# Kernel optimization log

Measured on AMD Instinct MI355X. Metric: run time of the kernel, lower is better.

The kernel has to match this reference:

```python
import jax, jax.numpy as jnp
import numpy as np

EPS = 1e-06

def phi(x):
    # canonical linear-attention feature map: elu(x) + 1 (positive features)
    return jax.nn.elu(x) + 1.0

def setup_inputs() -> dict:
    key = jax.random.key(0)
    kq, kk, kv = jax.random.split(key, 3)
    B, H, S, D = 4, 16, 4096, 64
    query = jax.random.normal(kq, (B, H, S, D), dtype=jnp.float32)
    k = jax.random.normal(kk, (B, H, S, D), dtype=jnp.float32)
    value = jax.random.normal(kv, (B, H, S, D), dtype=jnp.float32)
    attention_mask = jnp.ones((B, S), dtype=jnp.float32)
    return {"query": query, "key": k, "value": value, "attention_mask": attention_mask}

def reference(query, key, value, attention_mask):
    B, H, S, D = query.shape
    q = query / jnp.sqrt(jnp.asarray(D, query.dtype))
    phi_q = phi(q)                                   # [b,h,n,d]
    phi_k = phi(key)                                 # [b,h,n,d]
    mask = attention_mask[:, None, :, None].astype(phi_k.dtype)  # [b,1,n,1]
    phi_k = phi_k * mask
    kv_term = jnp.einsum('bhnd,bhnv->bhdv', phi_k, value)        # [b,h,d,v]
    output = jnp.einsum('bhnd,bhdv->bhnv', phi_q, kv_term)       # [b,h,n,v]
    k_one = jnp.sum(phi_k, axis=2)                               # [b,h,d] == phi_k @ masked ones
    normalizer = jnp.einsum('bhnd,bhd->bhn', phi_q, k_one)[..., None]  # [b,h,n,1]
    return output / (normalizer + EPS)
```

## Files before the change

kernel.cpp:

```cpp
#include <hip/hip_runtime.h>

typedef unsigned short ushort_t;
typedef unsigned int uint32;
typedef __bf16 bf16x8 __attribute__((ext_vector_type(8)));
typedef float f32x4 __attribute__((ext_vector_type(4)));

#define NB 4
#define NH 16
#define NS 4096
#define ND 64
#define NBH 64
#define EPSF 1e-6f

#define CH1 16
#define ROWS1 (NS / CH1)
#define P2R 64
#define LDJ 72
#define LDJW 36
#define BTSZ (80 * 64)

__device__ __forceinline__ float phi_f(float x) {
    return x > 0.0f ? x + 1.0f : __expf(x);
}
__device__ __forceinline__ ushort_t bf16_rn(float x) {
    uint32 u = __float_as_uint(x);
    uint32 r = (u + 0x7FFFu + ((u >> 16) & 1u)) >> 16;
    return (ushort_t)r;
}
__device__ __forceinline__ void split2(float x, ushort_t& h, ushort_t& l) {
    h = bf16_rn(x);
    float hf = __uint_as_float(((uint32)h) << 16);
    l = bf16_rn(x - hf);
}
union FragP { ushort_t s[8]; bf16x8 v; };
__device__ __forceinline__ bf16x8 ld_frag(const ushort_t* arr, int widx) {
    return *(const bf16x8*)((const uint32*)arr + widx);
}
__device__ __forceinline__ f32x4 mfma16(bf16x8 a, bf16x8 b, f32x4 c) {
    return __builtin_amdgcn_mfma_f32_16x16x32_bf16(a, b, c, 0, 0, 0);
}

template<bool PART>
__global__ __launch_bounds__(512, 8)
void la_pass1(const float* __restrict__ Kin, const float* __restrict__ Vin,
              const float* __restrict__ Min, float* __restrict__ okv,
              float* __restrict__ ok1)
{
    const int t  = threadIdx.x;
    const int cx = blockIdx.x;
    const int bh = blockIdx.y;
    const int bb = bh >> 4;
    const float* Kb = Kin + (long long)bh * NS * ND;
    const float* Vb = Vin + (long long)bh * NS * ND;
    const float* Mb = Min + (long long)bb * NS;

    __shared__ __align__(16) ushort_t skh[64 * LDJ], skl[64 * LDJ];
    __shared__ __align__(16) ushort_t svh[64 * LDJ], svl[64 * LDJ];

    const int p  = t & 31;
    const int c0 = (t >> 5) * 4;
    const int wv = t >> 6;
    const int ds = wv >> 1;
    const int nb = (wv & 1) * 2;
    const int m  = t & 15;
    const int q  = (t & 63) >> 4;

    const f32x4 zf = {0.f, 0.f, 0.f, 0.f};
    f32x4 acc0 = zf, acc1 = zf;
    float k1loc[4] = {0.f, 0.f, 0.f, 0.f};

    const int s0 = cx * ROWS1;

    float4 ka, kc, va, vc;
    float m0, m1;
#define LOADT(tt) { \
        const int r0_ = s0 + (tt) * 64 + 2 * p; \
        const float* kp_ = Kb + (long long)r0_ * ND + c0; \
        const float* vp_ = Vb + (long long)r0_ * ND + c0; \
        ka = *(const float4*)kp_;  kc = *(const float4*)(kp_ + ND); \
        va = *(const float4*)vp_;  vc = *(const float4*)(vp_ + ND); \
        m0 = Mb[r0_]; m1 = Mb[r0_ + 1]; }

    LOADT(0);

    for (int tile = 0; tile < ROWS1 / 64; ++tile) {
        __syncthreads();
        {
            const float kr0[4] = {ka.x, ka.y, ka.z, ka.w};
            const float kr1[4] = {kc.x, kc.y, kc.z, kc.w};
            const float vr0[4] = {va.x, va.y, va.z, va.w};
            const float vr1[4] = {vc.x, vc.y, vc.z, vc.w};
            #pragma unroll
            for (int i = 0; i < 4; ++i) {
                const float x0 = phi_f(kr0[i]) * m0;
                const float x1 = phi_f(kr1[i]) * m1;
                k1loc[i] += x0 + x1;
                ushort_t h0, l0, h1, l1;
                split2(x0, h0, l0); split2(x1, h1, l1);
                const int widx = (c0 + i) * LDJW + p;
                ((uint32*)skh)[widx] = (uint32)h0 | ((uint32)h1 << 16);
                ((uint32*)skl)[widx] = (uint32)l0 | ((uint32)l1 << 16);
                split2(vr0[i], h0, l0); split2(vr1[i], h1, l1);
                ((uint32*)svh)[widx] = (uint32)h0 | ((uint32)h1 << 16);
                ((uint32*)svl)[widx] = (uint32)l0 | ((uint32)l1 << 16);
            }
        }
        if (tile + 1 < ROWS1 / 64) LOADT(tile + 1);
        __syncthreads();
        #pragma unroll
        for (int ks = 0; ks < 2; ++ks) {
            const int fo = ks * 16 + q * 4;
            const bf16x8 ah = ld_frag(skh, (16 * ds + m) * LDJW + fo);
            const bf16x8 al = ld_frag(skl, (16 * ds + m) * LDJW + fo);
            {
                const bf16x8 fbh = ld_frag(svh, (16 * (nb + 0) + m) * LDJW + fo);
                const bf16x8 fbl = ld_frag(svl, (16 * (nb + 0) + m) * LDJW + fo);
                acc0 = mfma16(al, fbh, acc0); acc0 = mfma16(ah, fbl, acc0); acc0 = mfma16(ah, fbh, acc0);
            }
            {
                const bf16x8 fbh = ld_frag(svh, (16 * (nb + 1) + m) * LDJW + fo);
                const bf16x8 fbl = ld_frag(svl, (16 * (nb + 1) + m) * LDJW + fo);
                acc1 = mfma16(al, fbh, acc1); acc1 = mfma16(ah, fbl, acc1); acc1 = mfma16(ah, fbh, acc1);
            }
        }
    }
#undef LOADT

    const int dbase = 16 * ds + q * 4;
    if (PART) {
        float* outp = okv + (long long)(bh * CH1 + cx) * (ND * ND);
        #pragma unroll
        for (int i = 0; i < 4; ++i) {
            outp[(dbase + i) * ND + 16 * (nb + 0) + m] = acc0[i];
            outp[(dbase + i) * ND + 16 * (nb + 1) + m] = acc1[i];
        }
    } else {
        float* outp = okv + (long long)bh * (ND * ND);
        #pragma unroll
        for (int i = 0; i < 4; ++i) {
            atomicAdd(&outp[(dbase + i) * ND + 16 * (nb + 0) + m], acc0[i]);
            atomicAdd(&outp[(dbase + i) * ND + 16 * (nb + 1) + m], acc1[i]);
        }
    }
    __syncthreads();
    float* red = (float*)skh;
    #pragma unroll
    for (int i = 0; i < 4; ++i) red[(c0 + i) * 33 + p] = k1loc[i];
    __syncthreads();
    if (t < 64) {
        float s = 0.f;
        #pragma unroll
        for (int pp = 0; pp < 32; ++pp) s += red[t * 33 + pp];
        if (PART) ok1[(bh * CH1 + cx) * ND + t] = s;
        else      atomicAdd(&ok1[bh * ND + t], s);
    }
}

__global__ __launch_bounds__(256)
void la_reduce(const float* __restrict__ pkv, const float* __restrict__ pk1,
               ushort_t* __restrict__ BTh, ushort_t* __restrict__ BTl)
{
    const int t = threadIdx.x;
    const int bh = blockIdx.x;
    const float4* src = (const float4*)(pkv + (long long)bh * CH1 * ND * ND);
    float4 a[4];
    #pragma unroll
    for (int i = 0; i < 4; ++i) { a[i].x = 0.f; a[i].y = 0.f; a[i].z = 0.f; a[i].w = 0.f; }
    for (int c = 0; c < CH1; ++c) {
        #pragma unroll
        for (int i = 0; i < 4; ++i) {
            const float4 v = src[c * 1024 + t + 256 * i];
            a[i].x += v.x; a[i].y += v.y; a[i].z += v.z; a[i].w += v.w;
        }
    }
    ushort_t* oh = BTh + (long long)bh * BTSZ;
    ushort_t* ol = BTl + (long long)bh * BTSZ;
    #pragma unroll
    for (int i = 0; i < 4; ++i) {
        const int e4 = t + 256 * i;
        const int d  = e4 >> 4;
        const int v0 = (e4 & 15) * 4;
        const float vals[4] = {a[i].x, a[i].y, a[i].z, a[i].w};
        #pragma unroll
        for (int j = 0; j < 4; ++j) {
            ushort_t h, l; split2(vals[j], h, l);
            oh[(v0 + j) * ND + d] = h;
            ol[(v0 + j) * ND + d] = l;
        }
    }
    if (t < ND) {
        float s = 0.f;
        for (int c = 0; c < CH1; ++c) s += pk1[(bh * CH1 + c) * ND + t];
        ushort_t h, l; split2(s, h, l);
        oh[64 * ND + t] = h; ol[64 * ND + t] = l;
    }
    for (int z = t; z < 15 * 64; z += 256) { oh[65 * ND + z] = 0; ol[65 * ND + z] = 0; }
}

__global__ __launch_bounds__(256)
void la_convert(const float* __restrict__ kv, const float* __restrict__ k1,
                ushort_t* __restrict__ BTh, ushort_t* __restrict__ BTl)
{
    const int t = threadIdx.x;
    const int bh = blockIdx.x;
    const float* kvb = kv + (long long)bh * ND * ND;
    ushort_t* oh = BTh + (long long)bh * BTSZ;
    ushort_t* ol = BTl + (long long)bh * BTSZ;
    for (int e = t; e < ND * ND; e += 256) {
        const int d = e >> 6, v = e & 63;
        ushort_t h, l; split2(kvb[e], h, l);
        oh[v * ND + d] = h; ol[v * ND + d] = l;
    }
    if (t < ND) { ushort_t h, l; split2(k1[bh * ND + t], h, l); oh[64 * ND + t] = h; ol[64 * ND + t] = l; }
    for (int z = t; z < 15 * 64; z += 256) { oh[65 * ND + z] = 0; ol[65 * ND + z] = 0; }
}

__global__ __launch_bounds__(256, 6)
void la_pass2(const float* __restrict__ Qin, const ushort_t* __restrict__ BTh,
              const ushort_t* __restrict__ BTl, float* __restrict__ Out)
{
    const int t  = threadIdx.x;
    const int bh = blockIdx.y;
    const int s0 = blockIdx.x * P2R;
    const long long base = (long long)bh * NS * ND;
    const int wv = t >> 6;
    const int m  = t & 15;
    const int q  = (t & 63) >> 4;
    const int lane = t & 63;
    const ushort_t* Bh = BTh + (long long)bh * BTSZ;
    const ushort_t* Bl = BTl + (long long)bh * BTSZ;

    bf16x8 aH[2], aL[2];
    {
        const int row = s0 + 16 * wv + m;
        const float* qp = Qin + base + (long long)row * ND;
        float4 x0[2], x1[2];
        #pragma unroll
        for (int ks = 0; ks < 2; ++ks) {
            x0[ks] = *(const float4*)(qp + ks * 32 + q * 8);
            x1[ks] = *(const float4*)(qp + ks * 32 + q * 8 + 4);
        }
        #pragma unroll
        for (int ks = 0; ks < 2; ++ks) {
            const float xs[8] = {x0[ks].x, x0[ks].y, x0[ks].z, x0[ks].w,
                                 x1[ks].x, x1[ks].y, x1[ks].z, x1[ks].w};
            FragP fh, fl;
            #pragma unroll
            for (int i = 0; i < 8; ++i) {
                ushort_t h, l; split2(phi_f(xs[i] * 0.125f), h, l);
                fh.s[i] = h; fl.s[i] = l;
            }
            aH[ks] = fh.v; aL[ks] = fl.v;
        }
    }

    const f32x4 zf = {0.f, 0.f, 0.f, 0.f};
    f32x4 acc[5];
    #pragma unroll
    for (int b = 0; b < 5; ++b) acc[b] = zf;

    #pragma unroll
    for (int nt = 0; nt < 5; ++nt) {
        #pragma unroll
        for (int ks = 0; ks < 2; ++ks) {
            const int bo = (16 * nt + m) * ND + ks * 32 + q * 8;
            const bf16x8 fbh = *(const bf16x8*)(Bh + bo);
            const bf16x8 fbl = *(const bf16x8*)(Bl + bo);
            acc[nt] = mfma16(aL[ks], fbh, acc[nt]);
            acc[nt] = mfma16(aH[ks], fbl, acc[nt]);
            acc[nt] = mfma16(aH[ks], fbh, acc[nt]);
        }
    }

    float* outb = Out + base;
    const int rbase = s0 + 16 * wv + q * 4;
    #pragma unroll
    for (int i = 0; i < 4; ++i) {
        const float nv = __shfl(acc[4][i], lane & 48, 64);
        const float rn = 1.0f / (nv + EPSF);
        const long long ro = (long long)(rbase + i) * ND;
        outb[ro +  0 + m] = acc[0][i] * rn;
        outb[ro + 16 + m] = acc[1][i] * rn;
        outb[ro + 32 + m] = acc[2][i] * rn;
        outb[ro + 48 + m] = acc[3][i] * rn;
    }
}

extern "C" void kernel_launch(void* const* d_in, const int* in_sizes, int n_in,
                              void* d_out, int out_size, void* d_ws, size_t ws_size,
                              hipStream_t stream)
{
    const float* Q = (const float*)d_in[0];
    const float* K = (const float*)d_in[1];
    const float* V = (const float*)d_in[2];
    const float* M = (const float*)d_in[3];
    float* Out = (float*)d_out;

    const size_t partf = (size_t)NBH * CH1 * ND * ND;
    const size_t pk1f  = (size_t)NBH * CH1 * ND;
    const size_t kvf   = (size_t)NBH * ND * ND;
    const size_t k1f   = (size_t)NBH * ND;
    const size_t btu   = (size_t)NBH * BTSZ;
    const size_t need  = (partf + pk1f) * sizeof(float) + 2 * btu * sizeof(ushort_t);

    if (ws_size >= need) {
        float* PKV = (float*)d_ws;
        float* PK1 = PKV + partf;
        ushort_t* BThp = (ushort_t*)(PK1 + pk1f);
        ushort_t* BTlp = BThp + btu;
        la_pass1<true><<<dim3(CH1, NBH), dim3(512), 0, stream>>>(K, V, M, PKV, PK1);
        la_reduce<<<dim3(NBH), dim3(256), 0, stream>>>(PKV, PK1, BThp, BTlp);
        la_pass2<<<dim3(NS / P2R, NBH), dim3(256), 0, stream>>>(Q, BThp, BTlp, Out);
    } else {
        float* KVb = (float*)d_ws;
        float* K1b = KVb + kvf;
        ushort_t* BThp = (ushort_t*)(K1b + k1f);
        ushort_t* BTlp = BThp + btu;
        hipMemsetAsync(d_ws, 0, (kvf + k1f) * sizeof(float), stream);
        la_pass1<false><<<dim3(CH1, NBH), dim3(512), 0, stream>>>(K, V, M, KVb, K1b);
        la_convert<<<dim3(NBH), dim3(256), 0, stream>>>(KVb, K1b, BThp, BTlp);
        la_pass2<<<dim3(NS / P2R, NBH), dim3(256), 0, stream>>>(Q, BThp, BTlp, Out);
    }
}
```

Measured before the change: 264.9 us.

## Restructure pass1 to 256 threads with four accumulators per wave

```diff
diff --git a/kernel.cpp b/kernel.cpp
--- a/kernel.cpp
+++ b/kernel.cpp
@@ -15,8 +15,8 @@
 #define CH1 16
 #define ROWS1 (NS / CH1)
 #define P2R 64
-#define LDJ 72
-#define LDJW 36
+#define LDJ 70
+#define LDJW 35
 #define BTSZ (80 * 64)
 
 __device__ __forceinline__ float phi_f(float x) {
@@ -32,16 +32,23 @@
     float hf = __uint_as_float(((uint32)h) << 16);
     l = bf16_rn(x - hf);
 }
+union FragU { uint32 u[4]; bf16x8 v; };
+__device__ __forceinline__ bf16x8 ld_frag(const ushort_t* arr, int widx) {
+    const uint32* p = (const uint32*)arr;
+    FragU f;
+    f.u[0] = p[widx]; f.u[1] = p[widx + 1]; f.u[2] = p[widx + 2]; f.u[3] = p[widx + 3];
+    return f.v;
+}
 union FragP { ushort_t s[8]; bf16x8 v; };
-__device__ __forceinline__ bf16x8 ld_frag(const ushort_t* arr, int widx) {
-    return *(const bf16x8*)((const uint32*)arr + widx);
+__device__ __forceinline__ bf16x8 ld_frag16(const ushort_t* arr, int off16) {
+    return *(const bf16x8*)(arr + off16);
 }
 __device__ __forceinline__ f32x4 mfma16(bf16x8 a, bf16x8 b, f32x4 c) {
     return __builtin_amdgcn_mfma_f32_16x16x32_bf16(a, b, c, 0, 0, 0);
 }
 
 template<bool PART>
-__global__ __launch_bounds__(512, 8)
+__global__ __launch_bounds__(256, 4)
 void la_pass1(const float* __restrict__ Kin, const float* __restrict__ Vin,
               const float* __restrict__ Min, float* __restrict__ okv,
               float* __restrict__ ok1)
@@ -57,52 +64,50 @@
     __shared__ __align__(16) ushort_t skh[64 * LDJ], skl[64 * LDJ];
     __shared__ __align__(16) ushort_t svh[64 * LDJ], svl[64 * LDJ];
 
-    const int p  = t & 31;
-    const int c0 = (t >> 5) * 4;
-    const int wv = t >> 6;
-    const int ds = wv >> 1;
-    const int nb = (wv & 1) * 2;
-    const int m  = t & 15;
-    const int q  = (t & 63) >> 4;
+    const int rr0 = t >> 4;
+    const int c   = (t & 15) * 4;
+    const int wv  = t >> 6;
+    const int m   = t & 15;
+    const int q   = (t & 63) >> 4;
 
     const f32x4 zf = {0.f, 0.f, 0.f, 0.f};
-    f32x4 acc0 = zf, acc1 = zf;
+    f32x4 acc0 = zf, acc1 = zf, acc2 = zf, acc3 = zf;
     float k1loc[4] = {0.f, 0.f, 0.f, 0.f};
 
     const int s0 = cx * ROWS1;
 
-    float4 ka, kc, va, vc;
-    float m0, m1;
+    float4 k4[4], v4[4];
+    float  mk[4];
 #define LOADT(tt) { \
-        const int r0_ = s0 + (tt) * 64 + 2 * p; \
-        const float* kp_ = Kb + (long long)r0_ * ND + c0; \
-        const float* vp_ = Vb + (long long)r0_ * ND + c0; \
-        ka = *(const float4*)kp_;  kc = *(const float4*)(kp_ + ND); \
-        va = *(const float4*)vp_;  vc = *(const float4*)(vp_ + ND); \
-        m0 = Mb[r0_]; m1 = Mb[r0_ + 1]; }
+        const long long rb_ = (long long)(s0 + (tt) * 64 + rr0); \
+        const float* kp_ = Kb + rb_ * ND + c; \
+        const float* vp_ = Vb + rb_ * ND + c; \
+        k4[0] = *(const float4*)(kp_);            v4[0] = *(const float4*)(vp_); \
+        k4[1] = *(const float4*)(kp_ + 16 * ND);  v4[1] = *(const float4*)(vp_ + 16 * ND); \
+        k4[2] = *(const float4*)(kp_ + 32 * ND);  v4[2] = *(const float4*)(vp_ + 32 * ND); \
+        k4[3] = *(const float4*)(kp_ + 48 * ND);  v4[3] = *(const float4*)(vp_ + 48 * ND); \
+        mk[0] = Mb[rb_]; mk[1] = Mb[rb_ + 16]; mk[2] = Mb[rb_ + 32]; mk[3] = Mb[rb_ + 48]; }
 
     LOADT(0);
 
     for (int tile = 0; tile < ROWS1 / 64; ++tile) {
         __syncthreads();
-        {
-            const float kr0[4] = {ka.x, ka.y, ka.z, ka.w};
-            const float kr1[4] = {kc.x, kc.y, kc.z, kc.w};
-            const float vr0[4] = {va.x, va.y, va.z, va.w};
-            const float vr1[4] = {vc.x, vc.y, vc.z, vc.w};
+        #pragma unroll
+        for (int j = 0; j < 4; ++j) {
+            const int rr = rr0 + 16 * j;
+            const float xs[4] = {k4[j].x, k4[j].y, k4[j].z, k4[j].w};
+            const float vs[4] = {v4[j].x, v4[j].y, v4[j].z, v4[j].w};
             #pragma unroll
             for (int i = 0; i < 4; ++i) {
-                const float x0 = phi_f(kr0[i]) * m0;
-                const float x1 = phi_f(kr1[i]) * m1;
-                k1loc[i] += x0 + x1;
-                ushort_t h0, l0, h1, l1;
-                split2(x0, h0, l0); split2(x1, h1, l1);
-                const int widx = (c0 + i) * LDJW + p;
-                ((uint32*)skh)[widx] = (uint32)h0 | ((uint32)h1 << 16);
-                ((uint32*)skl)[widx] = (uint32)l0 | ((uint32)l1 << 16);
-                split2(vr0[i], h0, l0); split2(vr1[i], h1, l1);
-                ((uint32*)svh)[widx] = (uint32)h0 | ((uint32)h1 << 16);
-                ((uint32*)svl)[widx] = (uint32)l0 | ((uint32)l1 << 16);
+                const float x = phi_f(xs[i]) * mk[j];
+                k1loc[i] += x;
+                ushort_t h, l;
+                split2(x, h, l);
+                skh[(c + i) * LDJ + rr] = h;
+                skl[(c + i) * LDJ + rr] = l;
+                split2(vs[i], h, l);
+                svh[(c + i) * LDJ + rr] = h;
+                svl[(c + i) * LDJ + rr] = l;
             }
         }
         if (tile + 1 < ROWS1 / 64) LOADT(tile + 1);
@@ -110,47 +115,61 @@
         #pragma unroll
         for (int ks = 0; ks < 2; ++ks) {
             const int fo = ks * 16 + q * 4;
-            const bf16x8 ah = ld_frag(skh, (16 * ds + m) * LDJW + fo);
-            const bf16x8 al = ld_frag(skl, (16 * ds + m) * LDJW + fo);
+            const bf16x8 ah = ld_frag(skh, (16 * wv + m) * LDJW + fo);
+            const bf16x8 al = ld_frag(skl, (16 * wv + m) * LDJW + fo);
             {
-                const bf16x8 fbh = ld_frag(svh, (16 * (nb + 0) + m) * LDJW + fo);
-                const bf16x8 fbl = ld_frag(svl, (16 * (nb + 0) + m) * LDJW + fo);
+                const bf16x8 fbh = ld_frag(svh, (0 + m) * LDJW + fo);
+                const bf16x8 fbl = ld_frag(svl, (0 + m) * LDJW + fo);
                 acc0 = mfma16(al, fbh, acc0); acc0 = mfma16(ah, fbl, acc0); acc0 = mfma16(ah, fbh, acc0);
             }
             {
-                const bf16x8 fbh = ld_frag(svh, (16 * (nb + 1) + m) * LDJW + fo);
-                const bf16x8 fbl = ld_frag(svl, (16 * (nb + 1) + m) * LDJW + fo);
+                const bf16x8 fbh = ld_frag(svh, (16 + m) * LDJW + fo);
+                const bf16x8 fbl = ld_frag(svl, (16 + m) * LDJW + fo);
                 acc1 = mfma16(al, fbh, acc1); acc1 = mfma16(ah, fbl, acc1); acc1 = mfma16(ah, fbh, acc1);
             }
+            {
+                const bf16x8 fbh = ld_frag(svh, (32 + m) * LDJW + fo);
+                const bf16x8 fbl = ld_frag(svl, (32 + m) * LDJW + fo);
+                acc2 = mfma16(al, fbh, acc2); acc2 = mfma16(ah, fbl, acc2); acc2 = mfma16(ah, fbh, acc2);
+            }
+            {
+                const bf16x8 fbh = ld_frag(svh, (48 + m) * LDJW + fo);
+                const bf16x8 fbl = ld_frag(svl, (48 + m) * LDJW + fo);
+                acc3 = mfma16(al, fbh, acc3); acc3 = mfma16(ah, fbl, acc3); acc3 = mfma16(ah, fbh, acc3);
+            }
         }
     }
 #undef LOADT
 
-    const int dbase = 16 * ds + q * 4;
+    const int dbase = 16 * wv + q * 4;
     if (PART) {
         float* outp = okv + (long long)(bh * CH1 + cx) * (ND * ND);
         #pragma unroll
         for (int i = 0; i < 4; ++i) {
-            outp[(dbase + i) * ND + 16 * (nb + 0) + m] = acc0[i];
-            outp[(dbase + i) * ND + 16 * (nb + 1) + m] = acc1[i];
+            outp[(dbase + i) * ND +  0 + m] = acc0[i];
+            outp[(dbase + i) * ND + 16 + m] = acc1[i];
+            outp[(dbase + i) * ND + 32 + m] = acc2[i];
+            outp[(dbase + i) * ND + 48 + m] = acc3[i];
         }
     } else {
         float* outp = okv + (long long)bh * (ND * ND);
         #pragma unroll
         for (int i = 0; i < 4; ++i) {
-            atomicAdd(&outp[(dbase + i) * ND + 16 * (nb + 0) + m], acc0[i]);
-            atomicAdd(&outp[(dbase + i) * ND + 16 * (nb + 1) + m], acc1[i]);
+            atomicAdd(&outp[(dbase + i) * ND +  0 + m], acc0[i]);
+            atomicAdd(&outp[(dbase + i) * ND + 16 + m], acc1[i]);
+            atomicAdd(&outp[(dbase + i) * ND + 32 + m], acc2[i]);
+            atomicAdd(&outp[(dbase + i) * ND + 48 + m], acc3[i]);
         }
     }
     __syncthreads();
     float* red = (float*)skh;
     #pragma unroll
-    for (int i = 0; i < 4; ++i) red[(c0 + i) * 33 + p] = k1loc[i];
+    for (int i = 0; i < 4; ++i) red[(c + i) * 17 + rr0] = k1loc[i];
     __syncthreads();
     if (t < 64) {
         float s = 0.f;
         #pragma unroll
-        for (int pp = 0; pp < 32; ++pp) s += red[t * 33 + pp];
+        for (int g = 0; g < 16; ++g) s += red[t * 17 + g];
         if (PART) ok1[(bh * CH1 + cx) * ND + t] = s;
         else      atomicAdd(&ok1[bh * ND + t], s);
     }
@@ -264,8 +283,8 @@
         #pragma unroll
         for (int ks = 0; ks < 2; ++ks) {
             const int bo = (16 * nt + m) * ND + ks * 32 + q * 8;
-            const bf16x8 fbh = *(const bf16x8*)(Bh + bo);
-            const bf16x8 fbl = *(const bf16x8*)(Bl + bo);
+            const bf16x8 fbh = ld_frag16(Bh, bo);
+            const bf16x8 fbl = ld_frag16(Bl, bo);
             acc[nt] = mfma16(aL[ks], fbh, acc[nt]);
             acc[nt] = mfma16(aH[ks], fbl, acc[nt]);
             acc[nt] = mfma16(aH[ks], fbh, acc[nt]);
@@ -308,7 +327,7 @@
         float* PK1 = PKV + partf;
         ushort_t* BThp = (ushort_t*)(PK1 + pk1f);
         ushort_t* BTlp = BThp + btu;
-        la_pass1<true><<<dim3(CH1, NBH), dim3(512), 0, stream>>>(K, V, M, PKV, PK1);
+        la_pass1<true><<<dim3(CH1, NBH), dim3(256), 0, stream>>>(K, V, M, PKV, PK1);
         la_reduce<<<dim3(NBH), dim3(256), 0, stream>>>(PKV, PK1, BThp, BTlp);
         la_pass2<<<dim3(NS / P2R, NBH), dim3(256), 0, stream>>>(Q, BThp, BTlp, Out);
     } else {
@@ -317,7 +336,7 @@
         ushort_t* BThp = (ushort_t*)(K1b + k1f);
         ushort_t* BTlp = BThp + btu;
         hipMemsetAsync(d_ws, 0, (kvf + k1f) * sizeof(float), stream);
-        la_pass1<false><<<dim3(CH1, NBH), dim3(512), 0, stream>>>(K, V, M, KVb, K1b);
+        la_pass1<false><<<dim3(CH1, NBH), dim3(256), 0, stream>>>(K, V, M, KVb, K1b);
         la_convert<<<dim3(NBH), dim3(256), 0, stream>>>(KVb, K1b, BThp, BTlp);
         la_pass2<<<dim3(NS / P2R, NBH), dim3(256), 0, stream>>>(Q, BThp, BTlp, Out);
     }
```

After: 257.3 us. -2.9%, faster.
